# Kernel tuning notes

Measured on AMD Instinct MI355X. Metric: run time of the kernel, lower is better.

Reference implementation:

```python
import math
import jax, jax.numpy as jnp
import numpy as np

B, L = 2, 4096
D_MODEL, D_STATE, D_CONV, EXPAND = 1024, 64, 4, 2
D_INNER = EXPAND * D_MODEL
DT_RANK = max(1, D_MODEL // 16)
EPS = float(jnp.finfo(jnp.float32).eps)  # torch nn.RMSNorm default eps


def setup_inputs() -> dict:
    key = jax.random.key(0)
    ks = jax.random.split(key, 8)
    sc = lambda k, shape, scale: jax.random.normal(k, shape, jnp.float32) * scale
    x = jax.random.normal(ks[0], (B, L, D_MODEL), jnp.float32)
    in_proj_w = sc(ks[1], (2 * D_INNER, D_MODEL), D_MODEL ** -0.5)
    conv_w = sc(ks[2], (D_INNER, 1, D_CONV), D_CONV ** -0.5)  # depthwise kernel
    conv_b = jnp.zeros((D_INNER,), jnp.float32)
    norm_w = jnp.ones((D_INNER,), jnp.float32)
    dt_std = DT_RANK ** -0.5
    dt_w = jax.random.uniform(ks[3], (D_INNER, D_INNER), jnp.float32, -dt_std, dt_std)
    dt_b = jnp.full((D_INNER,), math.log(0.5), jnp.float32)
    A_log = jnp.log(jnp.tile(jnp.arange(1, D_STATE + 1, dtype=jnp.float32), (D_INNER, 1)))
    D = jnp.ones((D_INNER,), jnp.float32)
    B_w = sc(ks[4], (D_STATE, D_INNER), D_INNER ** -0.5)
    C_w = sc(ks[5], (D_STATE, D_INNER), D_INNER ** -0.5)
    out_w = sc(ks[6], (D_MODEL, D_INNER), D_INNER ** -0.5)
    return dict(x=x, in_proj_w=in_proj_w, conv_w=conv_w, conv_b=conv_b,
                norm_w=norm_w, dt_w=dt_w, dt_b=dt_b, A_log=A_log, D=D,
                B_w=B_w, C_w=C_w, out_w=out_w)


def _mamba2_fwd(x, in_proj_w, conv_w, conv_b, norm_w, dt_w, dt_b, A_log, D, B_w, C_w, out_w):
    batch, seq_len, _ = x.shape
    # input projection + gating
    xg = x @ in_proj_w.T                               # [B, L, 2*d_inner]
    x_inner, gate = jnp.split(xg, 2, axis=-1)
    x_inner = x_inner * jax.nn.silu(gate)
    # causal depthwise conv1d (left pad d_conv-1, keep first L outputs)
    lhs = x_inner.transpose(0, 2, 1)                   # [B, d_inner, L]
    conv = jax.lax.conv_general_dilated(
        lhs, conv_w, window_strides=(1,), padding=[(D_CONV - 1, 0)],
        feature_group_count=conv_w.shape[0])
    x_conv = (conv + conv_b[None, :, None]).transpose(0, 2, 1)  # [B, L, d_inner]
    # RMSNorm
    x_conv = x_conv * jax.lax.rsqrt(jnp.mean(x_conv ** 2, axis=-1, keepdims=True) + EPS) * norm_w
    # SSM parameters
    dt = jax.nn.softplus(x_conv @ dt_w.T + dt_b)       # [B, L, d_inner]
    A = -jnp.exp(A_log)                                # [d_inner, d_state]
    Bt = x_conv @ B_w.T                                # [B, L, d_state]
    Ct = x_conv @ C_w.T                                # [B, L, d_state]

    # selective scan: h_t = exp(dt_t * A) * h_{t-1} + dt_t * B_t * x_t
    def step(h, inp):
        dt_t, b_t, c_t, xc_t = inp                     # [B,d], [B,N], [B,N], [B,d]
        A_bar = jnp.exp(dt_t[..., None] * A)           # [B, d_inner, d_state]
        h = A_bar * h + (dt_t * xc_t)[..., None] * b_t[:, None, :]
        y_t = jnp.einsum('bdn,bn->bd', h, c_t)
        return h, y_t

    h0 = jnp.zeros((batch, x_conv.shape[-1], D_STATE), x_conv.dtype)
    xs = (dt.transpose(1, 0, 2), Bt.transpose(1, 0, 2),
          Ct.transpose(1, 0, 2), x_conv.transpose(1, 0, 2))
    _, ys = jax.lax.scan(step, h0, xs)                 # ys: [L, B, d_inner]
    y = ys.transpose(1, 0, 2) + D * x_conv             # skip connection
    return y @ out_w.T                                 # [B, L, d_model]


def reference(x, in_proj_w, conv_w, conv_b, norm_w, dt_w, dt_b, A_log, D, B_w, C_w, out_w):
    return _mamba2_fwd(x, in_proj_w, conv_w, conv_b, norm_w, dt_w, dt_b, A_log, D, B_w, C_w, out_w)
```

## Files before the change

kernel.cpp:

```cpp
#include <hip/hip_runtime.h>
#include <cmath>

#define BB 2
#define LL 4096
#define DM 1024
#define DI 2048
#define NS 64
static constexpr float EPSF  = 1.1920928955078125e-07f;
static constexpr float LOG2E = 1.4426950408889634f;

typedef unsigned short u16;
typedef __attribute__((ext_vector_type(4))) unsigned short u16x4;
typedef __attribute__((ext_vector_type(8))) short bf16x8;
typedef __attribute__((ext_vector_type(4))) float f32x4;

__device__ __forceinline__ u16 f2bf(float f){
    unsigned u = __float_as_uint(f);
    return (u16)((u + 0x7fffu + ((u >> 16) & 1u)) >> 16);
}
__device__ __forceinline__ float bf2f(u16 h){ return __uint_as_float(((unsigned)h) << 16); }
__device__ __forceinline__ void gload16(const void* g, void* l){
    __builtin_amdgcn_global_load_lds((const __attribute__((address_space(1))) void*)g,
                                     (__attribute__((address_space(3))) void*)l, 16, 0, 0);
}

__global__ __launch_bounds__(256)
void cvt_all(const float* __restrict__ s0, const float* __restrict__ s1,
             const float* __restrict__ s2, const float* __restrict__ s3,
             const float* __restrict__ s4, const float* __restrict__ s5,
             u16* __restrict__ d0, u16* __restrict__ d1, u16* __restrict__ d2,
             u16* __restrict__ d3, u16* __restrict__ d4, u16* __restrict__ d5)
{
    size_t v = (size_t)blockIdx.x * 256 + threadIdx.x;
    const float* src; u16* dst; size_t off;
    int seg;
    if      (v < 2097152u){ src=s0; dst=d0; off=v; seg=0; }
    else if (v < 3145728u){ src=s1; dst=d1; off=v-2097152u; seg=1; }
    else if (v < 4194304u){ src=s2; dst=d2; off=v-3145728u; seg=2; }
    else if (v < 4227072u){ src=s3; dst=d3; off=v-4194304u; seg=3; }
    else if (v < 4259840u){ src=s4; dst=d4; off=v-4227072u; seg=4; }
    else                  { src=s5; dst=d5; off=v-4259840u; seg=5; }
    size_t i = off*4;
    size_t isrc = i;
    if (seg == 1){
        size_t r = i >> 10, c = i & 1023;
        size_t g = r >> 6, w6 = r & 63;
        size_t s = (w6 < 32) ? (g*32 + w6) : (2048 + g*32 + (w6 - 32));
        isrc = s*1024 + c;
    }
    float4 x = *(const float4*)(src+isrc);
    u16x4 o; o[0]=f2bf(x.x); o[1]=f2bf(x.y); o[2]=f2bf(x.z); o[3]=f2bf(x.w);
    *(u16x4*)(dst+i) = o;
}

template<int EPI>
__global__ __launch_bounds__(512)
void gemm256(const u16* __restrict__ A, const u16* __restrict__ W,
             const float* __restrict__ bias, u16* __restrict__ out,
             int M, int N, int K)
{
    __shared__ u16 Adb[2][256*64];
    __shared__ u16 Bdb[2][256*64];
    const int tid  = threadIdx.x;
    const int lane = tid & 63;
    const int w    = tid >> 6;
    const int n0 = blockIdx.x * 256;
    const int m0 = blockIdx.y * 256;
    const int NT = K >> 6;

    f32x4 acc[2][16];
    #pragma unroll
    for (int mf=0; mf<2; mf++)
        #pragma unroll
        for (int nf=0; nf<16; nf++)
            #pragma unroll
            for (int r=0;r<4;r++) acc[mf][nf][r] = 0.f;

    auto stageA = [&](int kt, int buf){
        const int k0 = kt << 6;
        #pragma unroll
        for (int i=0;i<4;i++){
            const int s = i*512 + tid;
            const int row = s >> 3;
            const int q = (s & 7) ^ (row & 7);
            gload16(A + (size_t)(m0+row)*K + k0 + q*8, &Adb[buf][s*8]);
        }
    };
    auto stageBh = [&](int kt, int nh, int buf){
        const int k0 = kt << 6;
        #pragma unroll
        for (int i=0;i<2;i++){
            const int s = i*512 + tid;
            const int row = nh*128 + (s >> 3);
            const int q = (s & 7) ^ (row & 7);
            gload16(W + (size_t)(n0+row)*K + k0 + q*8, &Bdb[buf][nh*8192 + s*8]);
        }
    };

    bf16x8 af[2][2];
    bf16x8 bfr[8];
    auto readA = [&](int ks, int buf){
        #pragma unroll
        for (int mf=0; mf<2; mf++){
            const int row = w*32 + mf*16 + (lane & 15);
            const int q = (ks*4 + (lane >> 4)) ^ (row & 7);
            af[ks][mf] = *(const bf16x8*)(&Adb[buf][row*64 + q*8]);
        }
    };
    auto readB = [&](int nh, int ks, int buf){
        #pragma unroll
        for (int nf=0; nf<8; nf++){
            const int row = nh*128 + nf*16 + (lane & 15);
            const int q = (ks*4 + (lane >> 4)) ^ (row & 7);
            bfr[nf] = *(const bf16x8*)(&Bdb[buf][row*64 + q*8]);
        }
    };
    auto mfma16 = [&](int nbase, int ks){
        __builtin_amdgcn_s_setprio(1);
        #pragma unroll
        for (int nf=0; nf<8; nf++)
            #pragma unroll
            for (int mf=0; mf<2; mf++)
                acc[mf][nbase+nf] = __builtin_amdgcn_mfma_f32_16x16x32_bf16(
                    af[ks][mf], bfr[nf], acc[mf][nbase+nf], 0,0,0);
        __builtin_amdgcn_s_setprio(0);
    };

    stageA(0, 0); stageBh(0, 0, 0); stageBh(0, 1, 0);

    int cur = 0;
    for (int kt = 0; kt < NT; ++kt){
        const int nb = cur ^ 1;
        const bool pre = (kt + 1 < NT);
        if (pre) asm volatile("s_waitcnt vmcnt(2)" ::: "memory");
        else     asm volatile("s_waitcnt vmcnt(0)" ::: "memory");
        __builtin_amdgcn_s_barrier();
        if (pre) stageA(kt+1, nb);
        readA(0, cur); readB(0, 0, cur);
        mfma16(0, 0);
        if (pre) asm volatile("s_waitcnt vmcnt(4)" ::: "memory");
        __builtin_amdgcn_s_barrier();
        if (pre) stageBh(kt+1, 0, nb);
        readB(1, 0, cur);
        mfma16(8, 0);
        __builtin_amdgcn_s_barrier();
        if (pre) stageBh(kt+1, 1, nb);
        readA(1, cur); readB(0, 1, cur);
        mfma16(0, 1);
        __builtin_amdgcn_s_barrier();
        readB(1, 1, cur);
        mfma16(8, 1);
        cur = nb;
    }

    if (EPI == 0){
        #pragma unroll
        for (int mf=0; mf<2; mf++)
            #pragma unroll
            for (int g4=0; g4<4; g4++)
                #pragma unroll
                for (int nf2=0; nf2<2; nf2++){
                    const int na = g4*4 + nf2;
                    const int d  = (n0 >> 1) + g4*32 + nf2*16 + (lane & 15);
                    #pragma unroll
                    for (int rj=0; rj<4; rj++){
                        const int m = m0 + w*32 + mf*16 + (lane >> 4)*4 + rj;
                        float v = acc[mf][na][rj];
                        float g = acc[mf][na+2][rj];
                        v = v * (g / (1.f + __expf(-g)));
                        out[(size_t)m*DI + d] = f2bf(v);
                    }
                }
    } else {
        #pragma unroll
        for (int mf=0; mf<2; mf++)
            #pragma unroll
            for (int na=0; na<16; na++){
                const int col = n0 + na*16 + (lane & 15);
                u16x4 o;
                #pragma unroll
                for (int rj=0; rj<4; rj++){
                    float z = acc[mf][na][rj] + bias[col];
                    float v = (z > 20.f) ? z : log1pf(__expf(z));
                    o[rj] = f2bf(v);
                }
                const int rb = m0 + w*32 + mf*16 + (lane >> 4)*4;
                const int bb = rb >> 12;
                const int l  = rb & (LL-1);
                *(u16x4*)(out + ((size_t)bb*DI + col)*LL + l) = o;
            }
    }
}

template<int MODE>
__global__ __launch_bounds__(256)
void gemm_bf16(const u16* __restrict__ A, const u16* __restrict__ W,
               void* __restrict__ Cout, int M, int N, int K)
{
    __shared__ u16 As[128*32];
    __shared__ u16 Bs[128*32];

    const int tid  = threadIdx.x;
    const int lane = tid & 63;
    const int wave = tid >> 6;
    const int m0 = blockIdx.y * 128;
    const int n0 = blockIdx.x * 128;
    const int wr = wave >> 1, wc = wave & 1;

    f32x4 acc[4][4];
    #pragma unroll
    for (int i=0;i<4;i++)
        #pragma unroll
        for (int j=0;j<4;j++)
            #pragma unroll
            for (int r=0;r<4;r++) acc[i][j][r] = 0.f;

    for (int k0 = 0; k0 < K; k0 += 32) {
        #pragma unroll
        for (int it = 0; it < 2; ++it) {
            const int s  = it*256 + tid;
            const int r  = s >> 2;
            const int q  = s & 3;
            const int qs = q ^ ((r >> 1) & 3);
            const int ub = (it*256 + wave*64) * 8;
            gload16(A + (size_t)(m0 + r)*K + k0 + qs*8, As + ub);
            gload16(W + (size_t)(n0 + r)*K + k0 + qs*8, Bs + ub);
        }
        __syncthreads();

        bf16x8 af[4], bfr[4];
        #pragma unroll
        for (int mi=0; mi<4; ++mi){
            const int r  = wr*64 + mi*16 + (lane & 15);
            const int qs = (lane >> 4) ^ ((r >> 1) & 3);
            af[mi] = *(const bf16x8*)(As + (r*4 + qs)*8);
        }
        #pragma unroll
        for (int ni=0; ni<4; ++ni){
            const int c  = wc*64 + ni*16 + (lane & 15);
            const int qs = (lane >> 4) ^ ((c >> 1) & 3);
            bfr[ni] = *(const bf16x8*)(Bs + (c*4 + qs)*8);
        }
        #pragma unroll
        for (int mi=0; mi<4; ++mi)
            #pragma unroll
            for (int ni=0; ni<4; ++ni)
                acc[mi][ni] = __builtin_amdgcn_mfma_f32_16x16x32_bf16(af[mi], bfr[ni], acc[mi][ni], 0,0,0);
        __syncthreads();
    }

    #pragma unroll
    for (int mi=0; mi<4; ++mi){
        #pragma unroll
        for (int ni=0; ni<4; ++ni){
            const int col = n0 + wc*64 + ni*16 + (lane & 15);
            #pragma unroll
            for (int rj=0; rj<4; ++rj){
                const int row = m0 + wr*64 + mi*16 + (lane >> 4)*4 + rj;
                float v = acc[mi][ni][rj];
                if (MODE==3)
                    ((float*)Cout)[((size_t)row*64 + (col & 63))*2 + (col >> 6)] = v;
                else
                    ((float*)Cout)[(size_t)row*N + col] = v;
            }
        }
    }
}

__global__ __launch_bounds__(256)
void conv_rms(const u16* __restrict__ xin, const float* __restrict__ cw,
              const float* __restrict__ cb, const float* __restrict__ nw,
              u16* __restrict__ xc)
{
    const int bl  = blockIdx.x;
    const int l   = bl & (LL-1);
    const int tid = threadIdx.x;
    const int d0  = tid * 8;

    float a[8];
    #pragma unroll
    for (int j=0;j<8;j++) a[j] = cb[d0+j];
    #pragma unroll
    for (int t=0;t<4;t++){
        const int ls = l - 3 + t;
        if (ls >= 0){
            bf16x8 xv = *(const bf16x8*)(xin + (size_t)(bl-3+t)*DI + d0);
            #pragma unroll
            for (int j=0;j<8;j++)
                a[j] += bf2f((u16)xv[j]) * cw[(d0+j)*4 + t];
        }
    }
    float ss = 0.f;
    #pragma unroll
    for (int j=0;j<8;j++) ss += a[j]*a[j];
    ss += __shfl_xor(ss,32); ss += __shfl_xor(ss,16); ss += __shfl_xor(ss,8);
    ss += __shfl_xor(ss,4);  ss += __shfl_xor(ss,2);  ss += __shfl_xor(ss,1);
    __shared__ float red[4];
    if ((tid & 63)==0) red[tid>>6] = ss;
    __syncthreads();
    const float tot   = red[0]+red[1]+red[2]+red[3];
    const float scale = rsqrtf(tot * (1.f/DI) + EPSF);
    u16x4 o0, o1;
    #pragma unroll
    for (int j=0;j<4;j++) o0[j] = f2bf(a[j]  *scale*nw[d0+j]);
    #pragma unroll
    for (int j=0;j<4;j++) o1[j] = f2bf(a[4+j]*scale*nw[d0+4+j]);
    *(u16x4*)(xc + (size_t)bl*DI + d0)     = o0;
    *(u16x4*)(xc + (size_t)bl*DI + d0 + 4) = o1;
}

__global__ __launch_bounds__(256)
void transpose_bf(const u16* __restrict__ in, u16* __restrict__ out, int R, int C)
{
    __shared__ u16 t[32][36];
    const int b  = blockIdx.z;
    const int r0 = blockIdx.y * 32;
    const int c0 = blockIdx.x * 32;
    const int ir = threadIdx.x >> 3;
    const int ic = (threadIdx.x & 7) * 4;
    const size_t base = (size_t)b * R * C;

    u16x4 v = *(const u16x4*)(in + base + (size_t)(r0+ir)*C + c0 + ic);
    #pragma unroll
    for (int k=0;k<4;k++) t[ir][ic+k] = v[k];
    __syncthreads();
    u16x4 o;
    #pragma unroll
    for (int k=0;k<4;k++) o[k] = t[ic+k][ir];
    *(u16x4*)(out + base + (size_t)(c0+ir)*R + r0 + ic) = o;
}

#define BSTAGE(MU) \
    { _Pragma("unroll") \
      for (int i=0;i<MU;i++){ \
          const bool g = (lane & MU) != 0; \
          float q = g ? p[i] : p[i+MU]; \
          float r = __shfl_xor(q, MU); \
          p[i] = (g ? p[i+MU] : p[i]) + r; \
      } }

__global__ __launch_bounds__(512)
void scan9(const u16* __restrict__ dtT, const u16* __restrict__ xcT,
           const float* __restrict__ BCi, const float* __restrict__ A_log,
           const float* __restrict__ Dp, u16* __restrict__ yT)
{
    __shared__ float lbc[2][64*128];
    __shared__ float dtu[8][64][2];
    const int tid  = threadIdx.x;
    const int lane = tid & 63;
    const int wave = tid >> 6;
    const int b    = blockIdx.x >> 8;
    const int d    = (blockIdx.x & 255) * 8 + wave;

    const float Ac = -__expf(A_log[d*NS + lane]) * LOG2E;
    const float Dd = Dp[d];
    const size_t chbase = ((size_t)b*DI + d) * LL;
    const u16* dtp = dtT + chbase;
    const u16* xcp = xcT + chbase;
    u16*       yp  = yT  + chbase;
    const float* bcb = BCi + (size_t)b * LL * 128;

    auto stage = [&](int t0, int bufi){
        const float* src = bcb + (size_t)t0 * 128;
        #pragma unroll
        for (int i=0;i<4;i++){
            const int slot = i*512 + wave*64;
            gload16(src + (size_t)(slot + lane)*4, &lbc[bufi][slot*4]);
        }
    };

    stage(0, 0);
    asm volatile("s_waitcnt vmcnt(0)" ::: "memory");
    __syncthreads();

    float h = 0.f;
    int cur = 0;
    for (int t0 = 0; t0 < LL; t0 += 64) {
        if (t0 + 64 < LL) stage(t0 + 64, cur ^ 1);

        const float dtL = bf2f(dtp[t0 + lane]);
        const float xcL = bf2f(xcp[t0 + lane]);
        *(float2*)&dtu[wave][lane][0] = make_float2(dtL, dtL * xcL);
        const float* lb = lbc[cur];
        const float* dub = &dtu[wave][0][0];

        float p[64];
        #pragma unroll
        for (int j=0;j<64;j++){
            const float2 du = *(const float2*)(dub + j*2);
            const float2 bc = *(const float2*)(lb + (j*64 + lane)*2);
            const float a   = exp2f(du.x * Ac);
            h = a*h + du.y*bc.x;
            p[j] = h * bc.y;
        }
        #pragma unroll
        for (int i=0;i<32;i++){
            float a0 = p[i], b0 = p[i+32];
            asm("v_permlane32_swap_b32 %0, %1" : "+v"(a0), "+v"(b0));
            p[i] = a0 + b0;
        }
        BSTAGE(16) BSTAGE(8) BSTAGE(4) BSTAGE(2) BSTAGE(1)
        {
            float yv = p[0] + Dd * xcL;
            unsigned pk;
            asm("v_cvt_pk_bf16_f32 %0, %1, %2" : "=v"(pk) : "v"(yv), "v"(yv));
            yp[t0 + lane] = (u16)pk;
        }

        asm volatile("s_waitcnt vmcnt(0)" ::: "memory");
        __syncthreads();
        cur ^= 1;
    }
}

extern "C" void kernel_launch(void* const* d_in, const int* in_sizes, int n_in,
                              void* d_out, int out_size, void* d_ws, size_t ws_size,
                              hipStream_t stream) {
    const float* x       = (const float*)d_in[0];
    const float* in_proj = (const float*)d_in[1];
    const float* conv_w  = (const float*)d_in[2];
    const float* conv_b  = (const float*)d_in[3];
    const float* norm_w  = (const float*)d_in[4];
    const float* dt_w    = (const float*)d_in[5];
    const float* dt_b    = (const float*)d_in[6];
    const float* A_log   = (const float*)d_in[7];
    const float* Dp      = (const float*)d_in[8];
    const float* B_w     = (const float*)d_in[9];
    const float* C_w     = (const float*)d_in[10];
    const float* out_w   = (const float*)d_in[11];

    const int M = BB * LL;
    u16* wsu = (u16*)d_ws;
    u16*   x_bf   = wsu;
    u16*   ip_bf  = wsu + (size_t)M*DM;
    u16*   dtw_bf = ip_bf + (size_t)2*DI*DM;
    u16*   bcw_bf = dtw_bf + (size_t)DI*DI;
    u16*   xin_bf = bcw_bf + (size_t)128*DI;
    u16*   xc_bf  = xin_bf + (size_t)M*DI;
    float* BC     = (float*)(xc_bf + (size_t)M*DI);
    u16*   ow_bf  = (u16*)(BC + (size_t)M*128);
    u16*   dtT_bf = xin_bf;
    u16*   xcT_bf = x_bf;
    u16*   yT_bf  = xc_bf;
    u16*   y_bf   = xin_bf;

    cvt_all<<<18688, 256, 0, stream>>>(x, in_proj, dt_w, B_w, C_w, out_w,
                                       x_bf, ip_bf, dtw_bf, bcw_bf,
                                       bcw_bf + (size_t)NS*DI, ow_bf);

    gemm256<0><<<dim3(2*DI/256, M/256), 512, 0, stream>>>(
        x_bf, ip_bf, nullptr, xin_bf, M, 2*DI, DM);

    conv_rms<<<M, 256, 0, stream>>>(xin_bf, conv_w, conv_b, norm_w, xc_bf);

    gemm256<1><<<dim3(DI/256, M/256), 512, 0, stream>>>(
        xc_bf, dtw_bf, dt_b, dtT_bf, M, DI, DI);

    gemm_bf16<3><<<dim3(1, M/128), 256, 0, stream>>>(
        xc_bf, bcw_bf, BC, M, 128, DI);

    transpose_bf<<<dim3(DI/32, LL/32, BB), 256, 0, stream>>>(xc_bf, xcT_bf, LL, DI);

    scan9<<<BB*DI/8, 512, 0, stream>>>(dtT_bf, xcT_bf, BC, A_log, Dp, yT_bf);

    transpose_bf<<<dim3(LL/32, DI/32, BB), 256, 0, stream>>>(yT_bf, y_bf, DI, LL);

    gemm_bf16<0><<<dim3(DM/128, M/128), 256, 0, stream>>>(
        y_bf, ow_bf, (float*)d_out, M, DM, DI);
}
```

Measured before the change: 936.3 us.

## Fuse B/C projection into dt GEMM, reuse gemm256 for out-proj, prefetch scan inputs

The B/C projection is folded into the dt GEMM by widening N to 2304. The extra column tiles read the B/C weights that sit right after dt_w in the workspace, and their epilogue writes the interleaved BC buffer. The separate low-parallelism 128-wide GEMM launch goes away, and xc is read once instead of twice. The output projection now runs on the 256x256 double-buffered gemm256 kernel instead of the simpler 128x128 one. The scan kernel loads the next tile's dt and xc values into registers one iteration early. Trade-offs: the bigger dt grid (288 blocks) can tile unevenly across CUs, the 256-wide output tiles give only 128 blocks for the out-proj, and the B/C weight buffer is padded to 256 rows of which half is unused.

```diff
diff --git a/kernel.cpp b/kernel.cpp
--- a/kernel.cpp
+++ b/kernel.cpp
@@ -56,8 +56,8 @@
 template<int EPI>
 __global__ __launch_bounds__(512)
 void gemm256(const u16* __restrict__ A, const u16* __restrict__ W,
-             const float* __restrict__ bias, u16* __restrict__ out,
-             int M, int N, int K)
+             const float* __restrict__ bias, void* __restrict__ outv,
+             float* __restrict__ bcout, int M, int N, int K)
 {
     __shared__ u16 Adb[2][256*64];
     __shared__ u16 Bdb[2][256*64];
@@ -154,6 +154,7 @@
     }
 
     if (EPI == 0){
+        u16* out = (u16*)outv;
         #pragma unroll
         for (int mf=0; mf<2; mf++)
             #pragma unroll
@@ -171,99 +172,52 @@
                         out[(size_t)m*DI + d] = f2bf(v);
                     }
                 }
+    } else if (EPI == 1){
+        u16* out = (u16*)outv;
+        if (n0 < 2048){
+            #pragma unroll
+            for (int mf=0; mf<2; mf++)
+                #pragma unroll
+                for (int na=0; na<16; na++){
+                    const int col = n0 + na*16 + (lane & 15);
+                    u16x4 o;
+                    #pragma unroll
+                    for (int rj=0; rj<4; rj++){
+                        float z = acc[mf][na][rj] + bias[col];
+                        float v = (z > 20.f) ? z : log1pf(__expf(z));
+                        o[rj] = f2bf(v);
+                    }
+                    const int rb = m0 + w*32 + mf*16 + (lane >> 4)*4;
+                    const int bb = rb >> 12;
+                    const int l  = rb & (LL-1);
+                    *(u16x4*)(out + ((size_t)bb*DI + col)*LL + l) = o;
+                }
+        } else {
+            #pragma unroll
+            for (int mf=0; mf<2; mf++)
+                #pragma unroll
+                for (int na=0; na<8; na++){
+                    const int n2 = na*16 + (lane & 15);
+                    #pragma unroll
+                    for (int rj=0; rj<4; rj++){
+                        const int row = m0 + w*32 + mf*16 + (lane >> 4)*4 + rj;
+                        bcout[((size_t)row*64 + (n2 & 63))*2 + (n2 >> 6)] = acc[mf][na][rj];
+                    }
+                }
+        }
     } else {
+        float* out = (float*)outv;
         #pragma unroll
         for (int mf=0; mf<2; mf++)
             #pragma unroll
             for (int na=0; na<16; na++){
                 const int col = n0 + na*16 + (lane & 15);
-                u16x4 o;
                 #pragma unroll
                 for (int rj=0; rj<4; rj++){
-                    float z = acc[mf][na][rj] + bias[col];
-                    float v = (z > 20.f) ? z : log1pf(__expf(z));
-                    o[rj] = f2bf(v);
+                    const int m = m0 + w*32 + mf*16 + (lane >> 4)*4 + rj;
+                    out[(size_t)m*N + col] = acc[mf][na][rj];
                 }
-                const int rb = m0 + w*32 + mf*16 + (lane >> 4)*4;
-                const int bb = rb >> 12;
-                const int l  = rb & (LL-1);
-                *(u16x4*)(out + ((size_t)bb*DI + col)*LL + l) = o;
             }
-    }
-}
-
-template<int MODE>
-__global__ __launch_bounds__(256)
-void gemm_bf16(const u16* __restrict__ A, const u16* __restrict__ W,
-               void* __restrict__ Cout, int M, int N, int K)
-{
-    __shared__ u16 As[128*32];
-    __shared__ u16 Bs[128*32];
-
-    const int tid  = threadIdx.x;
-    const int lane = tid & 63;
-    const int wave = tid >> 6;
-    const int m0 = blockIdx.y * 128;
-    const int n0 = blockIdx.x * 128;
-    const int wr = wave >> 1, wc = wave & 1;
-
-    f32x4 acc[4][4];
-    #pragma unroll
-    for (int i=0;i<4;i++)
-        #pragma unroll
-        for (int j=0;j<4;j++)
-            #pragma unroll
-            for (int r=0;r<4;r++) acc[i][j][r] = 0.f;
-
-    for (int k0 = 0; k0 < K; k0 += 32) {
-        #pragma unroll
-        for (int it = 0; it < 2; ++it) {
-            const int s  = it*256 + tid;
-            const int r  = s >> 2;
-            const int q  = s & 3;
-            const int qs = q ^ ((r >> 1) & 3);
-            const int ub = (it*256 + wave*64) * 8;
-            gload16(A + (size_t)(m0 + r)*K + k0 + qs*8, As + ub);
-            gload16(W + (size_t)(n0 + r)*K + k0 + qs*8, Bs + ub);
-        }
-        __syncthreads();
-
-        bf16x8 af[4], bfr[4];
-        #pragma unroll
-        for (int mi=0; mi<4; ++mi){
-            const int r  = wr*64 + mi*16 + (lane & 15);
-            const int qs = (lane >> 4) ^ ((r >> 1) & 3);
-            af[mi] = *(const bf16x8*)(As + (r*4 + qs)*8);
-        }
-        #pragma unroll
-        for (int ni=0; ni<4; ++ni){
-            const int c  = wc*64 + ni*16 + (lane & 15);
-            const int qs = (lane >> 4) ^ ((c >> 1) & 3);
-            bfr[ni] = *(const bf16x8*)(Bs + (c*4 + qs)*8);
-        }
-        #pragma unroll
-        for (int mi=0; mi<4; ++mi)
-            #pragma unroll
-            for (int ni=0; ni<4; ++ni)
-                acc[mi][ni] = __builtin_amdgcn_mfma_f32_16x16x32_bf16(af[mi], bfr[ni], acc[mi][ni], 0,0,0);
-        __syncthreads();
-    }
-
-    #pragma unroll
-    for (int mi=0; mi<4; ++mi){
-        #pragma unroll
-        for (int ni=0; ni<4; ++ni){
-            const int col = n0 + wc*64 + ni*16 + (lane & 15);
-            #pragma unroll
-            for (int rj=0; rj<4; ++rj){
-                const int row = m0 + wr*64 + mi*16 + (lane >> 4)*4 + rj;
-                float v = acc[mi][ni][rj];
-                if (MODE==3)
-                    ((float*)Cout)[((size_t)row*64 + (col & 63))*2 + (col >> 6)] = v;
-                else
-                    ((float*)Cout)[(size_t)row*N + col] = v;
-            }
-        }
     }
 }
 
@@ -370,16 +324,19 @@
     };
 
     stage(0, 0);
+    float dtL = bf2f(dtp[lane]);
+    float xcL = bf2f(xcp[lane]);
     asm volatile("s_waitcnt vmcnt(0)" ::: "memory");
     __syncthreads();
 
     float h = 0.f;
     int cur = 0;
     for (int t0 = 0; t0 < LL; t0 += 64) {
-        if (t0 + 64 < LL) stage(t0 + 64, cur ^ 1);
-
-        const float dtL = bf2f(dtp[t0 + lane]);
-        const float xcL = bf2f(xcp[t0 + lane]);
+        const bool more = (t0 + 64 < LL);
+        if (more) stage(t0 + 64, cur ^ 1);
+        float dtN = 0.f, xcN = 0.f;
+        if (more) { dtN = bf2f(dtp[t0 + 64 + lane]); xcN = bf2f(xcp[t0 + 64 + lane]); }
+
         *(float2*)&dtu[wave][lane][0] = make_float2(dtL, dtL * xcL);
         const float* lb = lbc[cur];
         const float* dub = &dtu[wave][0][0];
@@ -409,6 +366,7 @@
 
         asm volatile("s_waitcnt vmcnt(0)" ::: "memory");
         __syncthreads();
+        dtL = dtN; xcL = xcN;
         cur ^= 1;
     }
 }
@@ -435,7 +393,7 @@
     u16*   ip_bf  = wsu + (size_t)M*DM;
     u16*   dtw_bf = ip_bf + (size_t)2*DI*DM;
     u16*   bcw_bf = dtw_bf + (size_t)DI*DI;
-    u16*   xin_bf = bcw_bf + (size_t)128*DI;
+    u16*   xin_bf = bcw_bf + (size_t)256*DI;
     u16*   xc_bf  = xin_bf + (size_t)M*DI;
     float* BC     = (float*)(xc_bf + (size_t)M*DI);
     u16*   ow_bf  = (u16*)(BC + (size_t)M*128);
@@ -449,15 +407,12 @@
                                        bcw_bf + (size_t)NS*DI, ow_bf);
 
     gemm256<0><<<dim3(2*DI/256, M/256), 512, 0, stream>>>(
-        x_bf, ip_bf, nullptr, xin_bf, M, 2*DI, DM);
+        x_bf, ip_bf, nullptr, xin_bf, nullptr, M, 2*DI, DM);
 
     conv_rms<<<M, 256, 0, stream>>>(xin_bf, conv_w, conv_b, norm_w, xc_bf);
 
-    gemm256<1><<<dim3(DI/256, M/256), 512, 0, stream>>>(
-        xc_bf, dtw_bf, dt_b, dtT_bf, M, DI, DI);
-
-    gemm_bf16<3><<<dim3(1, M/128), 256, 0, stream>>>(
-        xc_bf, bcw_bf, BC, M, 128, DI);
+    gemm256<1><<<dim3(2304/256, M/256), 512, 0, stream>>>(
+        xc_bf, dtw_bf, dt_b, dtT_bf, BC, M, 2304, DI);
 
     transpose_bf<<<dim3(DI/32, LL/32, BB), 256, 0, stream>>>(xc_bf, xcT_bf, LL, DI);
 
@@ -465,6 +420,6 @@
 
     transpose_bf<<<dim3(LL/32, DI/32, BB), 256, 0, stream>>>(yT_bf, y_bf, DI, LL);
 
-    gemm_bf16<0><<<dim3(DM/128, M/128), 256, 0, stream>>>(
-        y_bf, ow_bf, (float*)d_out, M, DM, DI);
-}
+    gemm256<2><<<dim3(DM/256, M/256), 512, 0, stream>>>(
+        y_bf, ow_bf, nullptr, (float*)d_out, nullptr, M, DM, DI);
+}
```

Measured after the change: 1.042 ms. +11.3%, slower.
